# Performance work log

Measured on AMD Instinct MI355X. Metric: run time of the kernel, lower is better.

## Reference

```python
import jax, jax.numpy as jnp
import numpy as np

V, D, S, B = 32000, 1024, 2048, 4
H = 4 * D


def _sinusoidal_pe(max_len, d):
    position = np.arange(max_len, dtype=np.float32)[:, None]
    div_term = np.exp(np.arange(0, d, 2, dtype=np.float32) * (-np.log(10000.0) / d))
    pe = np.zeros((max_len, d), dtype=np.float32)
    pe[:, 0::2] = np.sin(position * div_term)
    pe[:, 1::2] = np.cos(position * div_term)
    return jnp.asarray(pe)


def setup_inputs() -> dict:
    key = jax.random.key(0)
    ks = jax.random.split(key, 13)
    std = 1.0 / np.sqrt(D)
    stdh = 1.0 / np.sqrt(H)
    w = lambda k, shp, s: (jax.random.normal(k, shp, jnp.float32) * s)
    inp = {
        "tokens": jax.random.randint(ks[0], (B, S), 0, V),
        "emb": jax.random.normal(ks[1], (V, D), jnp.float32),
        "pe": _sinusoidal_pe(S, D),
        "l1_wk": w(ks[2], (D, D), std),
        "l1_wv": w(ks[3], (D, D), std),
        "l1_wo": w(ks[4], (D, D), std),
        "l1_w1": w(ks[5], (D, H), std),
        "l1_w2": w(ks[6], (H, D), stdh),
        "l2_wk": w(ks[7], (D, D), std),
        "l2_wv": w(ks[8], (D, D), std),
        "l2_wo": w(ks[9], (D, D), std),
        "l2_w1": w(ks[10], (D, H), std),
        "l2_w2": w(ks[11], (H, D), stdh),
        "w_out": w(ks[12], (D, V), std),
    }
    return inp


def _block(h, mask, wk, wv, wo, w1, w2):
    d = h.shape[-1]
    xq = h                      # W_q is identity
    xk = h @ wk                 # [B,S,D]
    xv = h @ wv
    scores = jnp.einsum("bsd,btd->bst", xq, xk) / np.sqrt(float(d)) + mask
    attn = jax.nn.softmax(scores, axis=-1)          # [B,S,S]
    h_attn = jnp.einsum("bst,btd->bsd", attn, xv) @ wo
    h_res = h + h_attn
    h_ffn = jnp.maximum(h_res @ w1, 0.0) @ w2
    return h_res + h_ffn


def reference(tokens, emb, pe, l1_wk, l1_wv, l1_wo, l1_w1, l1_w2,
              l2_wk, l2_wv, l2_wo, l2_w1, l2_w2, w_out):
    seq_len = tokens.shape[1]
    h = emb[tokens] + pe[None, :seq_len, :]
    # causal additive mask: -inf above diagonal
    mask = jnp.triu(jnp.full((seq_len, seq_len), -jnp.inf, jnp.float32), k=1)
    h = _block(h, mask, l1_wk, l1_wv, l1_wo, l1_w1, l1_w2)
    h = _block(h, mask, l2_wk, l2_wv, l2_wo, l2_w1, l2_w2)
    logits = h[:, -1, :] @ w_out  # [B, V]
    return logits
```

## Files before the change

kernel.cpp:

```cpp
#include <hip/hip_runtime.h>

#define S_LEN 2048
#define D_DIM 1024
#define H_DIM 4096
#define V_DIM 32000
#define B_SZ  4

typedef float  f32x4  __attribute__((ext_vector_type(4)));
typedef __bf16 bf16x8 __attribute__((ext_vector_type(8)));

__device__ __forceinline__ ushort f2bf(float f) {
    union { float f; unsigned u; } v; v.f = f;
    unsigned r = v.u + 0x7fffu + ((v.u >> 16) & 1u);
    return (ushort)(r >> 16);
}

__global__ void bt_wtranspose(const float* __restrict__ in, ushort* __restrict__ out,
                              int R, int C) {
    __shared__ ushort s[64][65];
    int r0 = blockIdx.y * 64, c0 = blockIdx.x * 64;
    int t = threadIdx.x;
    int lr = t >> 2, lc4 = (t & 3) * 16;
    const float* src = in + (size_t)(r0 + lr) * C + c0 + lc4;
#pragma unroll
    for (int j = 0; j < 4; ++j) {
        float4 v = ((const float4*)src)[j];
        s[lr][lc4 + 4 * j + 0] = f2bf(v.x);
        s[lr][lc4 + 4 * j + 1] = f2bf(v.y);
        s[lr][lc4 + 4 * j + 2] = f2bf(v.z);
        s[lr][lc4 + 4 * j + 3] = f2bf(v.w);
    }
    __syncthreads();
    int oc = t >> 2, orr = (t & 3) * 16;
    ushort tmp[16] __attribute__((aligned(16)));
#pragma unroll
    for (int j = 0; j < 16; ++j) tmp[j] = s[orr + j][oc];
    ushort* dst = out + (size_t)(c0 + oc) * R + r0 + orr;
    *(uint4*)dst        = *(uint4*)tmp;
    *(uint4*)(dst + 8)  = *(uint4*)(tmp + 8);
}

__global__ void bt_transpose(const ushort* __restrict__ in, ushort* __restrict__ out,
                             int R, int C) {
    __shared__ ushort s[64][65];
    int r0 = blockIdx.y * 64, c0 = blockIdx.x * 64;
    int t = threadIdx.x;
    int lr = t >> 2, lc = (t & 3) * 16;
    const ushort* src = in + (size_t)(r0 + lr) * C + c0 + lc;
    uint4 v0 = ((const uint4*)src)[0];
    uint4 v1 = ((const uint4*)src)[1];
    ushort tin[16] __attribute__((aligned(16)));
    *(uint4*)tin = v0; *(uint4*)(tin + 8) = v1;
#pragma unroll
    for (int j = 0; j < 16; ++j) s[lr][lc + j] = tin[j];
    __syncthreads();
    int oc = t >> 2, orr = (t & 3) * 16;
    ushort tmp[16] __attribute__((aligned(16)));
#pragma unroll
    for (int j = 0; j < 16; ++j) tmp[j] = s[orr + j][oc];
    ushort* dst = out + (size_t)(c0 + oc) * R + r0 + orr;
    *(uint4*)dst       = *(uint4*)tmp;
    *(uint4*)(dst + 8) = *(uint4*)(tmp + 8);
}

__global__ void bt_embed(const int* __restrict__ tokens, const float* __restrict__ emb,
                         const float* __restrict__ pe, float* __restrict__ h,
                         ushort* __restrict__ hbf) {
    int row = blockIdx.x;
    int s   = row & (S_LEN - 1);
    int tok = tokens[row];
    int t   = threadIdx.x;
    float4 v = ((const float4*)(emb + (size_t)tok * D_DIM))[t];
    float4 p = ((const float4*)(pe + (size_t)s * D_DIM))[t];
    v.x += p.x; v.y += p.y; v.z += p.z; v.w += p.w;
    ((float4*)(h + (size_t)row * D_DIM))[t] = v;
    uint2 pk;
    pk.x = (unsigned)f2bf(v.x) | ((unsigned)f2bf(v.y) << 16);
    pk.y = (unsigned)f2bf(v.z) | ((unsigned)f2bf(v.w) << 16);
    ((uint2*)(hbf + (size_t)row * D_DIM))[t] = pk;
}

#define EPI_F32  0
#define EPI_BF16 1
#define EPI_RELU 2
#define EPI_RES  3

#define VMWAIT(N) asm volatile("s_waitcnt vmcnt(%0)" :: "n"(N) : "memory")
#define LGKM0()   asm volatile("s_waitcnt lgkmcnt(0)" ::: "memory")
#define SBAR()    __builtin_amdgcn_s_barrier()
#define SCHED0()  __builtin_amdgcn_sched_barrier(0)
#define AS1 __attribute__((address_space(1)))
#define AS3 __attribute__((address_space(3)))

template <int BM, int BN, int NW, int WCc, int EPI, bool CSKIP, bool KLIM, int SWZ>
__global__ __launch_bounds__(NW * 64, (NW == 8 ? 1 : 2))
void bt_gemm(const ushort* __restrict__ A, const ushort* __restrict__ B,
             float* Cf, ushort* Cb, const float* __restrict__ Res,
             int lda, int ldb, int ldc, int K,
             size_t strideA, size_t strideB, size_t strideC) {
    constexpr int WRr = NW / WCc;
    constexpr int MR  = BM / (16 * WRr);
    constexpr int NR  = BN / (16 * WCc);
    constexpr int MH  = MR / 2;
    constexpr int SLOT = (BM + BN) * 32;

    __shared__ ushort lds[4][SLOT];

    int bm, bn;
    if (SWZ == 1) {
        int gx = gridDim.x, gy = gridDim.y;
        int id = blockIdx.y * gx + blockIdx.x;
        int xcd = id & 7, slot = id >> 3;
        int bandH = gy >> 3;
        bm = xcd * bandH + (slot % bandH);
        bn = slot / bandH;
    } else if (SWZ == 2) {
        int gx = gridDim.x;
        int id = blockIdx.y * gx + blockIdx.x;
        int xcd = id & 7, slot = id >> 3;
        int bandW = gx >> 3;
        bn = xcd * bandW + (slot % bandW);
        bm = slot / bandW;
    } else { bm = blockIdx.y; bn = blockIdx.x; }

    if (CSKIP && bn * BN >= (bm + 1) * BM) return;

    const int tid  = threadIdx.x;
    const int lane = tid & 63;
    const int wid  = tid >> 6;
    const int wr   = wid / WCc, wc = wid % WCc;
    const int r15  = lane & 15, r4 = lane >> 4;
    const int lr   = lane >> 2;
    const int lsl  = lane & 3;
    const int kswz = (r4 ^ ((r15 >> 1) & 3)) * 8;

    const ushort* Ab = A + strideA * blockIdx.z + (size_t)bm * BM * lda;
    const ushort* Bb = B + strideB * blockIdx.z + (size_t)bn * BN * ldb;

    int NT = K >> 6;
    if (KLIM) { int lim = (bm + 1) * (BM / 64); if (lim < NT) NT = lim; }
    const int NH2 = 2 * NT;

    f32x4 acc[MR][NR];
#pragma unroll
    for (int m = 0; m < MR; ++m)
#pragma unroll
        for (int n = 0; n < NR; ++n) acc[m][n] = (f32x4){0.f, 0.f, 0.f, 0.f};

#define STAGE_PART(s_, p_)                                                        \
    {                                                                             \
        const int b_ = (s_) & 3;                                                  \
        const int c_ = lsl ^ ((lr >> 1) & 3);                                     \
        const int rw_ = (wid + (p_) * NW) * 16 + lr;                              \
        __builtin_amdgcn_global_load_lds(                                         \
            (const AS1 void*)(Ab + (size_t)(s_) * 32 + (size_t)rw_ * lda + c_ * 8), \
            (AS3 void*)(&lds[b_][0] + (wid + (p_) * NW) * 512), 16, 0, 0);        \
        __builtin_amdgcn_global_load_lds(                                         \
            (const AS1 void*)(Bb + (size_t)(s_) * 32 + (size_t)rw_ * ldb + c_ * 8), \
            (AS3 void*)(&lds[b_][BM * 32] + (wid + (p_) * NW) * 512), 16, 0, 0);  \
    }

#define PHASE(s_, mh_, DOSTAGE)                                                   \
    {                                                                             \
        const int b_ = (s_) & 3;                                                  \
        bf16x8 aq[MH], bq[NR];                                                    \
        _Pragma("unroll")                                                         \
        for (int mm = 0; mm < MH; ++mm) {                                         \
            int row = wr * (16 * MR) + ((mh_) * MH + mm) * 16 + r15;              \
            aq[mm] = *(const bf16x8*)(&lds[b_][row * 32 + kswz]);                 \
        }                                                                         \
        _Pragma("unroll")                                                         \
        for (int n = 0; n < NR; ++n) {                                            \
            int col = wc * (16 * NR) + n * 16 + r15;                              \
            bq[n] = *(const bf16x8*)(&lds[b_][BM * 32 + col * 32 + kswz]);        \
        }                                                                         \
        if (DOSTAGE) STAGE_PART((s_) + 3, mh_);                                   \
        SBAR();                                                                   \
        LGKM0(); SCHED0();                                                        \
        __builtin_amdgcn_s_setprio(1);                                            \
        _Pragma("unroll")                                                         \
        for (int mm = 0; mm < MH; ++mm)                                           \
            _Pragma("unroll")                                                     \
            for (int n = 0; n < NR; ++n)                                          \
                acc[(mh_) * MH + mm][n] =                                         \
                    __builtin_amdgcn_mfma_f32_16x16x32_bf16(aq[mm], bq[n],        \
                        acc[(mh_) * MH + mm][n], 0, 0, 0);                        \
        __builtin_amdgcn_s_setprio(0);                                            \
    }

    STAGE_PART(0, 0); STAGE_PART(0, 1);
    STAGE_PART(1, 0); STAGE_PART(1, 1);
    STAGE_PART(2, 0); STAGE_PART(2, 1);
    VMWAIT(8); SBAR();

    int s = 0;
    for (; s < NH2 - 3; ++s) {
        PHASE(s, 0, true);  SBAR();
        PHASE(s, 1, true);  VMWAIT(8); SBAR();
    }
    PHASE(s, 0, false); SBAR();
    PHASE(s, 1, false); VMWAIT(4); SBAR();
    ++s;
    PHASE(s, 0, false); SBAR();
    PHASE(s, 1, false); VMWAIT(0); SBAR();
    ++s;
    PHASE(s, 0, false); SBAR();
    PHASE(s, 1, false);

    size_t cz = strideC * blockIdx.z;
    const int rowb = bm * BM + wr * (16 * MR) + r4 * 4;
    const int colb = bn * BN + wc * (16 * NR) + r15;
#pragma unroll
    for (int m = 0; m < MR; ++m) {
#pragma unroll
        for (int r = 0; r < 4; ++r) {
            int row = rowb + m * 16 + r;
            size_t base = cz + (size_t)row * ldc + colb;
#pragma unroll
            for (int n = 0; n < NR; ++n) {
                float v = acc[m][n][r];
                size_t idx = base + n * 16;
                if (EPI == EPI_F32)       Cf[idx] = v;
                else if (EPI == EPI_BF16) Cb[idx] = f2bf(v);
                else if (EPI == EPI_RELU) Cb[idx] = f2bf(fmaxf(v, 0.f));
                else { float o = v + Res[idx]; Cf[idx] = o; Cb[idx] = f2bf(o); }
            }
        }
    }
#undef STAGE_PART
#undef PHASE
}

__device__ __forceinline__ float wred_max(float v) {
#pragma unroll
    for (int off = 32; off; off >>= 1) v = fmaxf(v, __shfl_xor(v, off));
    return v;
}
__device__ __forceinline__ float wred_sum(float v) {
#pragma unroll
    for (int off = 32; off; off >>= 1) v += __shfl_xor(v, off);
    return v;
}

__global__ void bt_softmax(const float* __restrict__ scores, ushort* __restrict__ probs) {
    int row = blockIdx.x;
    int s   = row & (S_LEN - 1);
    const float* src = scores + (size_t)row * S_LEN;
    ushort*      dst = probs  + (size_t)row * S_LEN;
    int tid = threadIdx.x;
    int nvalid = s + 1;

    float vals[8];
    float mx = -1e30f;
#pragma unroll
    for (int j = 0; j < 8; ++j) {
        int t = tid + j * 256;
        float v = (t < nvalid) ? src[t] * 0.03125f : -1e30f;
        vals[j] = v;
        mx = fmaxf(mx, v);
    }
    __shared__ float red[4], red2[4];
    mx = wred_max(mx);
    if ((tid & 63) == 0) red[tid >> 6] = mx;
    __syncthreads();
    mx = fmaxf(fmaxf(red[0], red[1]), fmaxf(red[2], red[3]));

    float sum = 0.f, ps[8];
#pragma unroll
    for (int j = 0; j < 8; ++j) {
        float p = exp2f((vals[j] - mx) * 1.44269504f);
        ps[j] = p; sum += p;
    }
    sum = wred_sum(sum);
    if ((tid & 63) == 0) red2[tid >> 6] = sum;
    __syncthreads();
    sum = red2[0] + red2[1] + red2[2] + red2[3];
    float inv = 1.0f / sum;
#pragma unroll
    for (int j = 0; j < 8; ++j) {
        int t = tid + j * 256;
        dst[t] = (t < nvalid) ? f2bf(ps[j] * inv) : (ushort)0;
    }
}

__global__ void bt_logits(const float* __restrict__ h, const float* __restrict__ wout,
                          float* __restrict__ out) {
    __shared__ float hl[4][128];
    int tid = threadIdx.x;
    int d0 = blockIdx.y * 128;
    if (tid < 128) {
#pragma unroll
        for (int b = 0; b < 4; ++b)
            hl[b][tid] = h[((size_t)b * S_LEN + (S_LEN - 1)) * D_DIM + d0 + tid];
    }
    __syncthreads();
    int v = blockIdx.x * 256 + tid;
    float a0 = 0, a1 = 0, a2 = 0, a3 = 0;
    for (int j = 0; j < 128; ++j) {
        float w = wout[(size_t)(d0 + j) * V_DIM + v];
        a0 += hl[0][j] * w; a1 += hl[1][j] * w;
        a2 += hl[2][j] * w; a3 += hl[3][j] * w;
    }
    atomicAdd(out + v, a0);
    atomicAdd(out + V_DIM + v, a1);
    atomicAdd(out + 2 * V_DIM + v, a2);
    atomicAdd(out + 3 * V_DIM + v, a3);
}

extern "C" void kernel_launch(void* const* d_in, const int* in_sizes, int n_in,
                              void* d_out, int out_size, void* d_ws, size_t ws_size,
                              hipStream_t stream) {
    const int*   tokens = (const int*)d_in[0];
    const float* emb    = (const float*)d_in[1];
    const float* pe     = (const float*)d_in[2];
    const float* wgt[10];
    for (int i = 0; i < 10; ++i) wgt[i] = (const float*)d_in[3 + i];
    const float* wout = (const float*)d_in[13];

    char* w = (char*)d_ws;
    size_t o = 0;
    auto take = [&](size_t sz) { char* p = w + o; o += (sz + 255) & ~(size_t)255; return p; };

    const size_t DD = (size_t)D_DIM * D_DIM * 2;
    const size_t DH = (size_t)D_DIM * H_DIM * 2;
    size_t wsz[10] = {DD, DD, DD, DH, DH, DD, DD, DD, DH, DH};
    ushort* wT[10];
    for (int i = 0; i < 10; ++i) wT[i] = (ushort*)take(wsz[i]);

    const size_t NROW = (size_t)B_SZ * S_LEN;
    float*  h0     = (float*)take(NROW * D_DIM * 4);
    float*  h1     = (float*)take(NROW * D_DIM * 4);
    ushort* hbf    = (ushort*)take(NROW * D_DIM * 2);
    ushort* hresbf = (ushort*)take(NROW * D_DIM * 2);
    ushort* xkbf   = (ushort*)take(NROW * D_DIM * 2);
    ushort* xvt    = (ushort*)take((size_t)D_DIM * NROW * 2);
    ushort* hattn  = (ushort*)take(NROW * D_DIM * 2);
    char*   G      = take((size_t)B_SZ * S_LEN * S_LEN * 4 + (size_t)B_SZ * S_LEN * S_LEN * 2);
    float*  scores = (float*)G;
    ushort* probs  = (ushort*)(G + (size_t)B_SZ * S_LEN * S_LEN * 4);
    ushort* tbf    = (ushort*)G;

    int wR[10] = {1024, 1024, 1024, 1024, 4096, 1024, 1024, 1024, 1024, 4096};
    int wC[10] = {1024, 1024, 1024, 4096, 1024, 1024, 1024, 1024, 4096, 1024};
    for (int i = 0; i < 10; ++i)
        bt_wtranspose<<<dim3(wC[i] / 64, wR[i] / 64), 256, 0, stream>>>(wgt[i], wT[i], wR[i], wC[i]);

    bt_embed<<<NROW, 256, 0, stream>>>(tokens, emb, pe, h0, hbf);

    auto layer = [&](ushort* wk, ushort* wv2, ushort* wo, ushort* w1, ushort* w2) {
        bt_gemm<128, 128, 4, 2, EPI_BF16, false, false, 1><<<dim3(8, 64), 256, 0, stream>>>(
            hbf, wk, nullptr, xkbf, nullptr, D_DIM, D_DIM, D_DIM, D_DIM, 0, 0, 0);
        bt_gemm<128, 128, 4, 2, EPI_BF16, false, false, 1><<<dim3(8, 64), 256, 0, stream>>>(
            hbf, wv2, nullptr, hresbf, nullptr, D_DIM, D_DIM, D_DIM, D_DIM, 0, 0, 0);
        bt_transpose<<<dim3(D_DIM / 64, NROW / 64), 256, 0, stream>>>(
            hresbf, xvt, (int)NROW, D_DIM);
        bt_gemm<128, 128, 4, 2, EPI_F32, true, false, 0><<<dim3(16, 16, B_SZ), 256, 0, stream>>>(
            hbf, xkbf, scores, nullptr, nullptr, D_DIM, D_DIM, S_LEN, D_DIM,
            (size_t)S_LEN * D_DIM, (size_t)S_LEN * D_DIM, (size_t)S_LEN * S_LEN);
        bt_softmax<<<NROW, 256, 0, stream>>>(scores, probs);
        bt_gemm<128, 128, 4, 2, EPI_BF16, false, true, 0><<<dim3(8, 16, B_SZ), 256, 0, stream>>>(
            probs, xvt, nullptr, hattn, nullptr, S_LEN, (int)NROW, D_DIM, S_LEN,
            (size_t)S_LEN * S_LEN, (size_t)S_LEN, (size_t)S_LEN * D_DIM);
        bt_gemm<128, 128, 4, 2, EPI_RES, false, false, 1><<<dim3(8, 64), 256, 0, stream>>>(
            hattn, wo, h1, hresbf, h0, D_DIM, D_DIM, D_DIM, D_DIM, 0, 0, 0);
        bt_gemm<256, 256, 8, 4, EPI_RELU, false, false, 1><<<dim3(16, 32), 512, 0, stream>>>(
            hresbf, w1, nullptr, tbf, nullptr, D_DIM, D_DIM, H_DIM, D_DIM, 0, 0, 0);
        bt_gemm<128, 128, 4, 2, EPI_RES, false, false, 1><<<dim3(8, 64), 256, 0, stream>>>(
            tbf, w2, h0, hbf, h1, H_DIM, H_DIM, D_DIM, H_DIM, 0, 0, 0);
    };
    layer(wT[0], wT[1], wT[2], wT[3], wT[4]);
    layer(wT[5], wT[6], wT[7], wT[8], wT[9]);

    hipMemsetAsync(d_out, 0, (size_t)B_SZ * V_DIM * sizeof(float), stream);
    bt_logits<<<dim3(V_DIM / 256, D_DIM / 128), 256, 0, stream>>>(h0, wout, (float*)d_out);
}
```

Measured before the change: 915.4 us.

## Fuse K/V projections into one GEMM and move all GEMMs to 512-thread tiles

Stores the transposed Wk and Wv weights side by side so K and V come from a single GEMM with N=2048 into an interleaved xkv buffer. The score GEMM reads K from it with a stride, and the transpose takes V from the column offset. Every GEMM now uses 8 waves with 256x256 or 256x128 tiles, and each B fragment is loaded from LDS once per k-step instead of once per half-phase. The goal is fewer launches, more data reuse per tile and fewer LDS reads. The cost is fewer blocks per GEMM, which can leave CUs underused on the smaller problems, plus higher register pressure.

Measured after the change: 838.4 us. -8.4%, faster.

```diff
diff --git a/kernel.cpp b/kernel.cpp
--- a/kernel.cpp
+++ b/kernel.cpp
@@ -41,12 +41,12 @@
 }
 
 __global__ void bt_transpose(const ushort* __restrict__ in, ushort* __restrict__ out,
-                             int R, int C) {
+                             int R, int ldin, int coff) {
     __shared__ ushort s[64][65];
     int r0 = blockIdx.y * 64, c0 = blockIdx.x * 64;
     int t = threadIdx.x;
     int lr = t >> 2, lc = (t & 3) * 16;
-    const ushort* src = in + (size_t)(r0 + lr) * C + c0 + lc;
+    const ushort* src = in + (size_t)(r0 + lr) * ldin + coff + c0 + lc;
     uint4 v0 = ((const uint4*)src)[0];
     uint4 v1 = ((const uint4*)src)[1];
     ushort tin[16] __attribute__((aligned(16)));
@@ -92,16 +92,18 @@
 #define AS1 __attribute__((address_space(1)))
 #define AS3 __attribute__((address_space(3)))
 
-template <int BM, int BN, int NW, int WCc, int EPI, bool CSKIP, bool KLIM, int SWZ>
-__global__ __launch_bounds__(NW * 64, (NW == 8 ? 1 : 2))
+template <int BM, int BN, int WRr, int WCc, int EPI, bool CSKIP, bool KLIM, int SWZ>
+__global__ __launch_bounds__(512, 2)
 void bt_gemm(const ushort* __restrict__ A, const ushort* __restrict__ B,
              float* Cf, ushort* Cb, const float* __restrict__ Res,
              int lda, int ldb, int ldc, int K,
              size_t strideA, size_t strideB, size_t strideC) {
-    constexpr int WRr = NW / WCc;
     constexpr int MR  = BM / (16 * WRr);
     constexpr int NR  = BN / (16 * WCc);
     constexpr int MH  = MR / 2;
+    constexpr int APARTS = BM / 128;
+    constexpr int BPARTS = BN / 128;
+    constexpr int LPS = APARTS + BPARTS;
     constexpr int SLOT = (BM + BN) * 32;
 
     __shared__ ushort lds[4][SLOT];
@@ -114,13 +116,6 @@
         int bandH = gy >> 3;
         bm = xcd * bandH + (slot % bandH);
         bn = slot / bandH;
-    } else if (SWZ == 2) {
-        int gx = gridDim.x;
-        int id = blockIdx.y * gx + blockIdx.x;
-        int xcd = id & 7, slot = id >> 3;
-        int bandW = gx >> 3;
-        bn = xcd * bandW + (slot % bandW);
-        bm = slot / bandW;
     } else { bm = blockIdx.y; bn = blockIdx.x; }
 
     if (CSKIP && bn * BN >= (bm + 1) * BM) return;
@@ -147,32 +142,37 @@
 #pragma unroll
         for (int n = 0; n < NR; ++n) acc[m][n] = (f32x4){0.f, 0.f, 0.f, 0.f};
 
+    bf16x8 bq[NR];
+
 #define STAGE_PART(s_, p_)                                                        \
     {                                                                             \
         const int b_ = (s_) & 3;                                                  \
         const int c_ = lsl ^ ((lr >> 1) & 3);                                     \
-        const int rw_ = (wid + (p_) * NW) * 16 + lr;                              \
+        const int rw_ = (wid + (p_) * 8) * 16 + lr;                               \
         __builtin_amdgcn_global_load_lds(                                         \
             (const AS1 void*)(Ab + (size_t)(s_) * 32 + (size_t)rw_ * lda + c_ * 8), \
-            (AS3 void*)(&lds[b_][0] + (wid + (p_) * NW) * 512), 16, 0, 0);        \
-        __builtin_amdgcn_global_load_lds(                                         \
-            (const AS1 void*)(Bb + (size_t)(s_) * 32 + (size_t)rw_ * ldb + c_ * 8), \
-            (AS3 void*)(&lds[b_][BM * 32] + (wid + (p_) * NW) * 512), 16, 0, 0);  \
+            (AS3 void*)(&lds[b_][0] + (wid + (p_) * 8) * 512), 16, 0, 0);         \
+        if (BPARTS == 2 || (p_) == 0)                                             \
+            __builtin_amdgcn_global_load_lds(                                     \
+                (const AS1 void*)(Bb + (size_t)(s_) * 32 + (size_t)rw_ * ldb + c_ * 8), \
+                (AS3 void*)(&lds[b_][BM * 32] + (wid + (p_) * 8) * 512), 16, 0, 0); \
     }
 
 #define PHASE(s_, mh_, DOSTAGE)                                                   \
     {                                                                             \
         const int b_ = (s_) & 3;                                                  \
-        bf16x8 aq[MH], bq[NR];                                                    \
+        bf16x8 aq[MH];                                                            \
+        if ((mh_) == 0) {                                                         \
+            _Pragma("unroll")                                                     \
+            for (int n = 0; n < NR; ++n) {                                        \
+                int col = wc * (16 * NR) + n * 16 + r15;                          \
+                bq[n] = *(const bf16x8*)(&lds[b_][BM * 32 + col * 32 + kswz]);    \
+            }                                                                     \
+        }                                                                         \
         _Pragma("unroll")                                                         \
         for (int mm = 0; mm < MH; ++mm) {                                         \
             int row = wr * (16 * MR) + ((mh_) * MH + mm) * 16 + r15;              \
             aq[mm] = *(const bf16x8*)(&lds[b_][row * 32 + kswz]);                 \
-        }                                                                         \
-        _Pragma("unroll")                                                         \
-        for (int n = 0; n < NR; ++n) {                                            \
-            int col = wc * (16 * NR) + n * 16 + r15;                              \
-            bq[n] = *(const bf16x8*)(&lds[b_][BM * 32 + col * 32 + kswz]);        \
         }                                                                         \
         if (DOSTAGE) STAGE_PART((s_) + 3, mh_);                                   \
         SBAR();                                                                   \
@@ -191,15 +191,15 @@
     STAGE_PART(0, 0); STAGE_PART(0, 1);
     STAGE_PART(1, 0); STAGE_PART(1, 1);
     STAGE_PART(2, 0); STAGE_PART(2, 1);
-    VMWAIT(8); SBAR();
+    VMWAIT(2 * LPS); SBAR();
 
     int s = 0;
     for (; s < NH2 - 3; ++s) {
         PHASE(s, 0, true);  SBAR();
-        PHASE(s, 1, true);  VMWAIT(8); SBAR();
+        PHASE(s, 1, true);  VMWAIT(2 * LPS); SBAR();
     }
     PHASE(s, 0, false); SBAR();
-    PHASE(s, 1, false); VMWAIT(4); SBAR();
+    PHASE(s, 1, false); VMWAIT(LPS); SBAR();
     ++s;
     PHASE(s, 0, false); SBAR();
     PHASE(s, 1, false); VMWAIT(0); SBAR();
@@ -313,8 +313,6 @@
     const int*   tokens = (const int*)d_in[0];
     const float* emb    = (const float*)d_in[1];
     const float* pe     = (const float*)d_in[2];
-    const float* wgt[10];
-    for (int i = 0; i < 10; ++i) wgt[i] = (const float*)d_in[3 + i];
     const float* wout = (const float*)d_in[13];
 
     char* w = (char*)d_ws;
@@ -323,16 +321,21 @@
 
     const size_t DD = (size_t)D_DIM * D_DIM * 2;
     const size_t DH = (size_t)D_DIM * H_DIM * 2;
-    size_t wsz[10] = {DD, DD, DD, DH, DH, DD, DD, DD, DH, DH};
-    ushort* wT[10];
-    for (int i = 0; i < 10; ++i) wT[i] = (ushort*)take(wsz[i]);
-
     const size_t NROW = (size_t)B_SZ * S_LEN;
+
+    ushort* wkvT[2]; ushort* woT[2]; ushort* w1T[2]; ushort* w2T[2];
+    for (int l = 0; l < 2; ++l) {
+        wkvT[l] = (ushort*)take(2 * DD);
+        woT[l]  = (ushort*)take(DD);
+        w1T[l]  = (ushort*)take(DH);
+        w2T[l]  = (ushort*)take(DH);
+    }
+
     float*  h0     = (float*)take(NROW * D_DIM * 4);
     float*  h1     = (float*)take(NROW * D_DIM * 4);
     ushort* hbf    = (ushort*)take(NROW * D_DIM * 2);
     ushort* hresbf = (ushort*)take(NROW * D_DIM * 2);
-    ushort* xkbf   = (ushort*)take(NROW * D_DIM * 2);
+    ushort* xkv    = (ushort*)take(NROW * 2 * D_DIM * 2);
     ushort* xvt    = (ushort*)take((size_t)D_DIM * NROW * 2);
     ushort* hattn  = (ushort*)take(NROW * D_DIM * 2);
     char*   G      = take((size_t)B_SZ * S_LEN * S_LEN * 4 + (size_t)B_SZ * S_LEN * S_LEN * 2);
@@ -340,36 +343,41 @@
     ushort* probs  = (ushort*)(G + (size_t)B_SZ * S_LEN * S_LEN * 4);
     ushort* tbf    = (ushort*)G;
 
-    int wR[10] = {1024, 1024, 1024, 1024, 4096, 1024, 1024, 1024, 1024, 4096};
-    int wC[10] = {1024, 1024, 1024, 4096, 1024, 1024, 1024, 1024, 4096, 1024};
-    for (int i = 0; i < 10; ++i)
-        bt_wtranspose<<<dim3(wC[i] / 64, wR[i] / 64), 256, 0, stream>>>(wgt[i], wT[i], wR[i], wC[i]);
+    for (int l = 0; l < 2; ++l) {
+        const float* wk = (const float*)d_in[3 + 5 * l + 0];
+        const float* wv = (const float*)d_in[3 + 5 * l + 1];
+        const float* wo = (const float*)d_in[3 + 5 * l + 2];
+        const float* w1 = (const float*)d_in[3 + 5 * l + 3];
+        const float* w2 = (const float*)d_in[3 + 5 * l + 4];
+        bt_wtranspose<<<dim3(16, 16), 256, 0, stream>>>(wk, wkvT[l], 1024, 1024);
+        bt_wtranspose<<<dim3(16, 16), 256, 0, stream>>>(wv, wkvT[l] + (size_t)D_DIM * D_DIM, 1024, 1024);
+        bt_wtranspose<<<dim3(16, 16), 256, 0, stream>>>(wo, woT[l], 1024, 1024);
+        bt_wtranspose<<<dim3(64, 16), 256, 0, stream>>>(w1, w1T[l], 1024, 4096);
+        bt_wtranspose<<<dim3(16, 64), 256, 0, stream>>>(w2, w2T[l], 4096, 1024);
+    }
 
     bt_embed<<<NROW, 256, 0, stream>>>(tokens, emb, pe, h0, hbf);
 
-    auto layer = [&](ushort* wk, ushort* wv2, ushort* wo, ushort* w1, ushort* w2) {
-        bt_gemm<128, 128, 4, 2, EPI_BF16, false, false, 1><<<dim3(8, 64), 256, 0, stream>>>(
-            hbf, wk, nullptr, xkbf, nullptr, D_DIM, D_DIM, D_DIM, D_DIM, 0, 0, 0);
-        bt_gemm<128, 128, 4, 2, EPI_BF16, false, false, 1><<<dim3(8, 64), 256, 0, stream>>>(
-            hbf, wv2, nullptr, hresbf, nullptr, D_DIM, D_DIM, D_DIM, D_DIM, 0, 0, 0);
-        bt_transpose<<<dim3(D_DIM / 64, NROW / 64), 256, 0, stream>>>(
-            hresbf, xvt, (int)NROW, D_DIM);
-        bt_gemm<128, 128, 4, 2, EPI_F32, true, false, 0><<<dim3(16, 16, B_SZ), 256, 0, stream>>>(
-            hbf, xkbf, scores, nullptr, nullptr, D_DIM, D_DIM, S_LEN, D_DIM,
-            (size_t)S_LEN * D_DIM, (size_t)S_LEN * D_DIM, (size_t)S_LEN * S_LEN);
+    auto layer = [&](int l) {
+        bt_gemm<256, 256, 2, 4, EPI_BF16, false, false, 1><<<dim3(8, 32), 512, 0, stream>>>(
+            hbf, wkvT[l], nullptr, xkv, nullptr, D_DIM, D_DIM, 2 * D_DIM, D_DIM, 0, 0, 0);
+        bt_transpose<<<dim3(16, 128), 256, 0, stream>>>(xkv, xvt, (int)NROW, 2 * D_DIM, D_DIM);
+        bt_gemm<256, 256, 2, 4, EPI_F32, true, false, 0><<<dim3(8, 8, B_SZ), 512, 0, stream>>>(
+            hbf, xkv, scores, nullptr, nullptr, D_DIM, 2 * D_DIM, S_LEN, D_DIM,
+            (size_t)S_LEN * D_DIM, (size_t)S_LEN * 2 * D_DIM, (size_t)S_LEN * S_LEN);
         bt_softmax<<<NROW, 256, 0, stream>>>(scores, probs);
-        bt_gemm<128, 128, 4, 2, EPI_BF16, false, true, 0><<<dim3(8, 16, B_SZ), 256, 0, stream>>>(
+        bt_gemm<256, 128, 4, 2, EPI_BF16, false, true, 0><<<dim3(8, 8, B_SZ), 512, 0, stream>>>(
             probs, xvt, nullptr, hattn, nullptr, S_LEN, (int)NROW, D_DIM, S_LEN,
             (size_t)S_LEN * S_LEN, (size_t)S_LEN, (size_t)S_LEN * D_DIM);
-        bt_gemm<128, 128, 4, 2, EPI_RES, false, false, 1><<<dim3(8, 64), 256, 0, stream>>>(
-            hattn, wo, h1, hresbf, h0, D_DIM, D_DIM, D_DIM, D_DIM, 0, 0, 0);
-        bt_gemm<256, 256, 8, 4, EPI_RELU, false, false, 1><<<dim3(16, 32), 512, 0, stream>>>(
-            hresbf, w1, nullptr, tbf, nullptr, D_DIM, D_DIM, H_DIM, D_DIM, 0, 0, 0);
-        bt_gemm<128, 128, 4, 2, EPI_RES, false, false, 1><<<dim3(8, 64), 256, 0, stream>>>(
-            tbf, w2, h0, hbf, h1, H_DIM, H_DIM, D_DIM, H_DIM, 0, 0, 0);
+        bt_gemm<256, 128, 4, 2, EPI_RES, false, false, 1><<<dim3(8, 32), 512, 0, stream>>>(
+            hattn, woT[l], h1, hresbf, h0, D_DIM, D_DIM, D_DIM, D_DIM, 0, 0, 0);
+        bt_gemm<256, 256, 2, 4, EPI_RELU, false, false, 1><<<dim3(16, 32), 512, 0, stream>>>(
+            hresbf, w1T[l], nullptr, tbf, nullptr, D_DIM, D_DIM, H_DIM, D_DIM, 0, 0, 0);
+        bt_gemm<256, 128, 4, 2, EPI_RES, false, false, 1><<<dim3(8, 32), 512, 0, stream>>>(
+            tbf, w2T[l], h0, hbf, h1, H_DIM, H_DIM, D_DIM, H_DIM, 0, 0, 0);
     };
-    layer(wT[0], wT[1], wT[2], wT[3], wT[4]);
-    layer(wT[5], wT[6], wT[7], wT[8], wT[9]);
+    layer(0);
+    layer(1);
 
     hipMemsetAsync(d_out, 0, (size_t)B_SZ * V_DIM * sizeof(float), stream);
     bt_logits<<<dim3(V_DIM / 256, D_DIM / 128), 256, 0, stream>>>(h0, wout, (float*)d_out);
```
